# Optimization experiments

Measured on AMD Instinct MI355X. Metric: run time of the kernel, lower is better.

The kernel has to match this reference:

```python
import jax, jax.numpy as jnp
import numpy as np

NUM_ITERATIONS = 3  # matches init kwarg num_iterations
B, R, CIN, COUT, K = 32, 2048, 64, 64, 16


def squash(s):
    # squash along the last (capsule-vector) axis, as in the torch module
    sq = jnp.sum(s * s, axis=-1, keepdims=True)
    return (sq / (1.0 + sq)) * s / jnp.sqrt(sq)


def setup_inputs() -> dict:
    key = jax.random.key(0)
    k1, k2 = jax.random.split(key)
    x = jax.random.normal(k1, (B, R, CIN), dtype=jnp.float32)
    route_weights = jax.random.normal(k2, (K, R, CIN, COUT), dtype=jnp.float32) * 0.05
    return {"x": x, "route_weights": route_weights}


def reference(x, route_weights):
    # priors[k,b,r,o] = sum_c x[b,r,c] * W[k,r,c,o]   -> [K, B, R, COUT]
    priors = jnp.einsum('brc,krco->kbro', x, route_weights)
    logits = jnp.zeros(priors.shape[:3] + (1,), dtype=priors.dtype)  # [K,B,R,1]
    outputs = None
    for i in range(NUM_ITERATIONS):
        probs = jax.nn.softmax(logits, axis=2)  # softmax over route nodes (torch dim=2)
        outputs = squash(jnp.sum(probs * priors, axis=2, keepdims=True))  # [K,B,1,COUT]
        if i != NUM_ITERATIONS - 1:
            logits = logits + jnp.sum(priors * outputs, axis=-1, keepdims=True)
    return outputs[:, :, 0, :]  # [K, B, COUT]
```

## Files before the change

### kernel.cpp

```cpp
#include <hip/hip_runtime.h>
#include <hip/hip_bf16.h>
#include <stdint.h>

#define NB 32
#define NR 2048
#define NC 64
#define NO 64
#define NK 16
#define CHC 8
#define NCHUNK (NC / CHC)

__device__ __forceinline__ uint32_t f2bf(float f) {
  uint32_t u = __builtin_bit_cast(uint32_t, f);
  return (u + 0x7fffu + ((u >> 16) & 1u)) >> 16;
}
__device__ __forceinline__ uint32_t packbf2(float lo, float hi) {
  return f2bf(lo) | (f2bf(hi) << 16);
}

__device__ __forceinline__ void gload_lds16(const float* g, float* l) {
  __builtin_amdgcn_global_load_lds(
      (const __attribute__((address_space(1))) void*)g,
      (__attribute__((address_space(3))) void*)l, 16, 0, 0);
}

__global__ __launch_bounds__(256) void transpose_x(const float* __restrict__ x,
                                                   float* __restrict__ xT) {
  __shared__ float tile[32][65];
  const int r = blockIdx.x, t = threadIdx.x;
  {
    const int b = t >> 3, c0 = (t & 7) << 3;
    const float* xp = x + ((size_t)b * NR + r) * NC + c0;
    float4 v0 = *(const float4*)xp;
    float4 v1 = *(const float4*)(xp + 4);
    tile[b][c0 + 0] = v0.x; tile[b][c0 + 1] = v0.y; tile[b][c0 + 2] = v0.z; tile[b][c0 + 3] = v0.w;
    tile[b][c0 + 4] = v1.x; tile[b][c0 + 5] = v1.y; tile[b][c0 + 6] = v1.z; tile[b][c0 + 7] = v1.w;
  }
  __syncthreads();
  {
    const int c = t >> 2, b0 = (t & 3) << 3;
    float4 w0 = make_float4(tile[b0 + 0][c], tile[b0 + 1][c], tile[b0 + 2][c], tile[b0 + 3][c]);
    float4 w1 = make_float4(tile[b0 + 4][c], tile[b0 + 5][c], tile[b0 + 6][c], tile[b0 + 7][c]);
    float* op = xT + ((size_t)r * NC + c) * NB + b0;
    *(float4*)op = w0;
    *(float4*)(op + 4) = w1;
  }
}

__global__ __launch_bounds__(256, 3) void priors_gemm(const float* __restrict__ xT,
                                                      const float* __restrict__ W,
                                                      __hip_bfloat16* __restrict__ priors) {
  __shared__ float ldsW[2][4][CHC][64];
  __shared__ float ldsX[2][4][CHC][32];
  const int w = threadIdx.x >> 6, lane = threadIdx.x & 63;
  const int bg = lane >> 3, og = lane & 7;
  const int k = blockIdx.x & 15;
  const int rbase = (blockIdx.x >> 4) * 4;
  const int r = rbase + w;

  const float* wsrc = W + ((size_t)(k * NR + rbase + (w >> 1))) * (NC * NO)
                        + (w & 1) * 256 + lane * 4;
  const float* xsrc = xT + ((size_t)r * NC) * NB + lane * 4;

  float acc[4][8] = {};

  auto stage = [&](int t, int buf) {
    const int c0 = t * CHC;
    float* dw = &ldsW[buf][0][0][0] + w * 256;
    gload_lds16(wsrc + c0 * 64, dw);
    gload_lds16(wsrc + (size_t)2 * (NC * NO) + c0 * 64, dw + 1024);
    gload_lds16(xsrc + c0 * 32, &ldsX[buf][0][0][0] + w * 256);
  };

  auto compute = [&](int buf) {
#pragma unroll
    for (int c = 0; c < CHC; ++c) {
      float4 xv = *(const float4*)&ldsX[buf][w][c][bg * 4];
      float4 wa = *(const float4*)&ldsW[buf][w][c][og * 8];
      float4 wb = *(const float4*)&ldsW[buf][w][c][og * 8 + 4];
      float xr[4] = {xv.x, xv.y, xv.z, xv.w};
      float wr[8] = {wa.x, wa.y, wa.z, wa.w, wb.x, wb.y, wb.z, wb.w};
#pragma unroll
      for (int a = 0; a < 4; ++a)
#pragma unroll
        for (int b = 0; b < 8; ++b) acc[a][b] = fmaf(xr[a], wr[b], acc[a][b]);
    }
  };

  stage(0, 0);
  __syncthreads();
#pragma unroll
  for (int t = 0; t < NCHUNK; ++t) {
    if (t + 1 < NCHUNK) stage(t + 1, (t + 1) & 1);
    compute(t & 1);
    __syncthreads();
  }

#pragma unroll
  for (int i = 0; i < 4; ++i) {
    uint4 uv;
    uv.x = packbf2(acc[i][0], acc[i][1]);
    uv.y = packbf2(acc[i][2], acc[i][3]);
    uv.z = packbf2(acc[i][4], acc[i][5]);
    uv.w = packbf2(acc[i][6], acc[i][7]);
    __hip_bfloat16* pp = priors + ((size_t)(k * NR + r) * NB + bg * 4 + i) * NO + og * 8;
    *(uint4*)pp = uv;
  }
}

template <int PASS>
__global__ __launch_bounds__(256) void routing(const __hip_bfloat16* __restrict__ priors,
                                               float* __restrict__ Abuf,
                                               const float* __restrict__ o_prev,
                                               float* __restrict__ o_out) {
  __shared__ float o_lds[64];
  __shared__ float red_num[4][8][8];
  __shared__ float red_den[4];
  const int kb = blockIdx.x;
  const int k = kb >> 5, b = kb & 31;
  const int tid = threadIdx.x, w = tid >> 6, lane = tid & 63;
  const int g = lane >> 3, sl = lane & 7;
  const int rsub = w * 8 + g;
  const __hip_bfloat16* pbase = priors + (size_t)k * NR * NB * NO + (size_t)b * NO;
  float* ab = Abuf + (size_t)kb * NR;

  if (PASS == 1) {
    float sum[8];
#pragma unroll
    for (int j = 0; j < 8; ++j) sum[j] = 0.f;
    for (int it = 0; it < NR / 32; ++it) {
      const int r = it * 32 + rsub;
      uint4 pv = *(const uint4*)(pbase + (size_t)r * (NB * NO) + sl * 8);
      sum[0] += __builtin_bit_cast(float, pv.x << 16);
      sum[1] += __builtin_bit_cast(float, pv.x & 0xffff0000u);
      sum[2] += __builtin_bit_cast(float, pv.y << 16);
      sum[3] += __builtin_bit_cast(float, pv.y & 0xffff0000u);
      sum[4] += __builtin_bit_cast(float, pv.z << 16);
      sum[5] += __builtin_bit_cast(float, pv.z & 0xffff0000u);
      sum[6] += __builtin_bit_cast(float, pv.w << 16);
      sum[7] += __builtin_bit_cast(float, pv.w & 0xffff0000u);
    }
#pragma unroll
    for (int m = 8; m < 64; m <<= 1)
#pragma unroll
      for (int j = 0; j < 8; ++j) sum[j] += __shfl_xor(sum[j], m, 64);
    if (lane < 8) {
#pragma unroll
      for (int j = 0; j < 8; ++j) red_num[w][lane][j] = sum[j];
    }
    __syncthreads();
    if (tid < 64) {
      const int s_ = tid >> 3, j_ = tid & 7;
      float sv = (red_num[0][s_][j_] + red_num[1][s_][j_] +
                  red_num[2][s_][j_] + red_num[3][s_][j_]) * (1.f / (float)NR);
      float sq = sv * sv;
#pragma unroll
      for (int m = 1; m < 64; m <<= 1) sq += __shfl_xor(sq, m, 64);
      o_lds[tid] = (sq / (1.f + sq)) * rsqrtf(sq) * sv;
    }
    __syncthreads();
  } else {
    if (tid < 64) o_lds[tid] = o_prev[kb * 64 + tid];
    __syncthreads();
  }

  float os[8];
#pragma unroll
  for (int j = 0; j < 8; ++j) os[j] = o_lds[sl * 8 + j];

  float num[8];
#pragma unroll
  for (int j = 0; j < 8; ++j) num[j] = 0.f;
  float den = 0.f;

  for (int it = 0; it < NR / 32; ++it) {
    const int r = it * 32 + rsub;
    uint4 pv = *(const uint4*)(pbase + (size_t)r * (NB * NO) + sl * 8);
    float f[8];
    f[0] = __builtin_bit_cast(float, pv.x << 16);
    f[1] = __builtin_bit_cast(float, pv.x & 0xffff0000u);
    f[2] = __builtin_bit_cast(float, pv.y << 16);
    f[3] = __builtin_bit_cast(float, pv.y & 0xffff0000u);
    f[4] = __builtin_bit_cast(float, pv.z << 16);
    f[5] = __builtin_bit_cast(float, pv.z & 0xffff0000u);
    f[6] = __builtin_bit_cast(float, pv.w << 16);
    f[7] = __builtin_bit_cast(float, pv.w & 0xffff0000u);

    float d = 0.f;
#pragma unroll
    for (int j = 0; j < 8; ++j) d = fmaf(f[j], os[j], d);
#pragma unroll
    for (int m = 1; m < 8; m <<= 1) d += __shfl_xor(d, m, 64);

    float lg;
    if (PASS == 1) {
      lg = d;
      if (sl == 0) ab[r] = d;
    } else {
      lg = d + ab[r];
    }
    float e = __expf(lg);
    den += e;
#pragma unroll
    for (int j = 0; j < 8; ++j) num[j] = fmaf(e, f[j], num[j]);
  }

#pragma unroll
  for (int m = 8; m < 64; m <<= 1) {
    den += __shfl_xor(den, m, 64);
#pragma unroll
    for (int j = 0; j < 8; ++j) num[j] += __shfl_xor(num[j], m, 64);
  }
  if (lane < 8) {
#pragma unroll
    for (int j = 0; j < 8; ++j) red_num[w][lane][j] = num[j];
    if (lane == 0) red_den[w] = den;
  }
  __syncthreads();

  if (tid < 64) {
    const int s_ = tid >> 3, j_ = tid & 7;
    float nm = red_num[0][s_][j_] + red_num[1][s_][j_] + red_num[2][s_][j_] + red_num[3][s_][j_];
    float dn = red_den[0] + red_den[1] + red_den[2] + red_den[3];
    float sv = nm / dn;
    float sq = sv * sv;
#pragma unroll
    for (int m = 1; m < 64; m <<= 1) sq += __shfl_xor(sq, m, 64);
    float ov = (sq / (1.f + sq)) * rsqrtf(sq) * sv;
    o_out[kb * 64 + tid] = ov;
  }
}

extern "C" void kernel_launch(void* const* d_in, const int* in_sizes, int n_in,
                              void* d_out, int out_size, void* d_ws, size_t ws_size,
                              hipStream_t stream) {
  const float* x = (const float*)d_in[0];
  const float* W = (const float*)d_in[1];
  float* out = (float*)d_out;
  char* ws = (char*)d_ws;

  size_t off = 0;
  float* xT = (float*)(ws + off);                  off += (size_t)NR * NC * NB * 4;
  __hip_bfloat16* priors = (__hip_bfloat16*)(ws + off); off += (size_t)NK * NB * NR * NO * 2;
  float* o1 = (float*)(ws + off);                  off += (size_t)NK * NB * NO * 4;
  float* Abuf = (float*)(ws + off);                off += (size_t)NK * NB * NR * 4;

  transpose_x<<<NR, 256, 0, stream>>>(x, xT);
  priors_gemm<<<(NR / 4) * NK, 256, 0, stream>>>(xT, W, priors);
  routing<1><<<NK * NB, 256, 0, stream>>>(priors, Abuf, nullptr, o1);
  routing<2><<<NK * NB, 256, 0, stream>>>(priors, Abuf, o1, out);
}
```

Measured before the change: 255.9 us.

## Compute priors with bf16 MFMA instead of scalar FP32 FMAs

The x transpose kernel now writes x pre-converted to bf16 in MFMA A-fragment layout. The priors GEMM is rewritten to stage W rows into LDS, convert them to bf16 B fragments on the fly, and run 16x16x32 bf16 MFMAs, with each wave handling one k and the block looping over 8 route nodes. The intent is to replace scalar FMA throughput with matrix-core throughput, since W is streamed once and the FMA work dominates. It adds bf16 rounding of the inputs, which costs precision, and adds an LDS round-trip epilogue for coalesced stores.

```diff
diff --git a/kernel.cpp b/kernel.cpp
--- a/kernel.cpp
+++ b/kernel.cpp
@@ -7,8 +7,9 @@
 #define NC 64
 #define NO 64
 #define NK 16
-#define CHC 8
-#define NCHUNK (NC / CHC)
+
+using bf16x8 = __attribute__((ext_vector_type(8))) short;
+using f32x4  = __attribute__((ext_vector_type(4))) float;
 
 __device__ __forceinline__ uint32_t f2bf(float f) {
   uint32_t u = __builtin_bit_cast(uint32_t, f);
@@ -24,87 +25,100 @@
       (__attribute__((address_space(3))) void*)l, 16, 0, 0);
 }
 
-__global__ __launch_bounds__(256) void transpose_x(const float* __restrict__ x,
-                                                   float* __restrict__ xT) {
-  __shared__ float tile[32][65];
+__global__ __launch_bounds__(256) void make_xbf(const float* __restrict__ x,
+                                                ushort* __restrict__ xbf) {
+  __shared__ float tile[32][72];
   const int r = blockIdx.x, t = threadIdx.x;
   {
     const int b = t >> 3, c0 = (t & 7) << 3;
     const float* xp = x + ((size_t)b * NR + r) * NC + c0;
-    float4 v0 = *(const float4*)xp;
-    float4 v1 = *(const float4*)(xp + 4);
-    tile[b][c0 + 0] = v0.x; tile[b][c0 + 1] = v0.y; tile[b][c0 + 2] = v0.z; tile[b][c0 + 3] = v0.w;
-    tile[b][c0 + 4] = v1.x; tile[b][c0 + 5] = v1.y; tile[b][c0 + 6] = v1.z; tile[b][c0 + 7] = v1.w;
+    *(float4*)&tile[b][c0] = *(const float4*)xp;
+    *(float4*)&tile[b][c0 + 4] = *(const float4*)(xp + 4);
   }
   __syncthreads();
   {
-    const int c = t >> 2, b0 = (t & 3) << 3;
-    float4 w0 = make_float4(tile[b0 + 0][c], tile[b0 + 1][c], tile[b0 + 2][c], tile[b0 + 3][c]);
-    float4 w1 = make_float4(tile[b0 + 4][c], tile[b0 + 5][c], tile[b0 + 6][c], tile[b0 + 7][c]);
-    float* op = xT + ((size_t)r * NC + c) * NB + b0;
-    *(float4*)op = w0;
-    *(float4*)(op + 4) = w1;
-  }
-}
-
-__global__ __launch_bounds__(256, 3) void priors_gemm(const float* __restrict__ xT,
+    const int ks = t >> 7, mt = (t >> 6) & 1, l = t & 63;
+    const int b = mt * 16 + (l & 15);
+    const int cb = ks * 32 + (l >> 4) * 8;
+    uint4 uv;
+    uv.x = packbf2(tile[b][cb + 0], tile[b][cb + 1]);
+    uv.y = packbf2(tile[b][cb + 2], tile[b][cb + 3]);
+    uv.z = packbf2(tile[b][cb + 4], tile[b][cb + 5]);
+    uv.w = packbf2(tile[b][cb + 6], tile[b][cb + 7]);
+    *(uint4*)(xbf + (size_t)r * 2048 + t * 8) = uv;
+  }
+}
+
+__global__ __launch_bounds__(256, 2) void priors_gemm(const ushort* __restrict__ xbf,
                                                       const float* __restrict__ W,
-                                                      __hip_bfloat16* __restrict__ priors) {
-  __shared__ float ldsW[2][4][CHC][64];
-  __shared__ float ldsX[2][4][CHC][32];
+                                                      ushort* __restrict__ priors) {
+  __shared__ float ldsW[2][4][2048];
   const int w = threadIdx.x >> 6, lane = threadIdx.x & 63;
-  const int bg = lane >> 3, og = lane & 7;
-  const int k = blockIdx.x & 15;
-  const int rbase = (blockIdx.x >> 4) * 4;
-  const int r = rbase + w;
-
-  const float* wsrc = W + ((size_t)(k * NR + rbase + (w >> 1))) * (NC * NO)
-                        + (w & 1) * 256 + lane * 4;
-  const float* xsrc = xT + ((size_t)r * NC) * NB + lane * 4;
-
-  float acc[4][8] = {};
-
-  auto stage = [&](int t, int buf) {
-    const int c0 = t * CHC;
-    float* dw = &ldsW[buf][0][0][0] + w * 256;
-    gload_lds16(wsrc + c0 * 64, dw);
-    gload_lds16(wsrc + (size_t)2 * (NC * NO) + c0 * 64, dw + 1024);
-    gload_lds16(xsrc + c0 * 32, &ldsX[buf][0][0][0] + w * 256);
+  const int g = lane >> 4, col = lane & 15;
+  const int kq = blockIdx.x & 3, rblk = blockIdx.x >> 2;
+  const int k = kq * 4 + w;
+
+  f32x4 acc[2][4];
+
+  auto stage = [&](int rr, int ks, int buf) {
+    const float* src = W + ((size_t)(k * NR + rblk * 8 + rr)) * 4096 + ks * 2048 + lane * 4;
+    float* dst = &ldsW[buf][w][0] + lane * 4;
+#pragma unroll
+    for (int i = 0; i < 8; ++i) gload_lds16(src + i * 256, dst + i * 256);
   };
 
-  auto compute = [&](int buf) {
-#pragma unroll
-    for (int c = 0; c < CHC; ++c) {
-      float4 xv = *(const float4*)&ldsX[buf][w][c][bg * 4];
-      float4 wa = *(const float4*)&ldsW[buf][w][c][og * 8];
-      float4 wb = *(const float4*)&ldsW[buf][w][c][og * 8 + 4];
-      float xr[4] = {xv.x, xv.y, xv.z, xv.w};
-      float wr[8] = {wa.x, wa.y, wa.z, wa.w, wb.x, wb.y, wb.z, wb.w};
-#pragma unroll
-      for (int a = 0; a < 4; ++a)
-#pragma unroll
-        for (int b = 0; b < 8; ++b) acc[a][b] = fmaf(xr[a], wr[b], acc[a][b]);
+  auto compute = [&](int rr, int ks, int buf) {
+    const float* pw = &ldsW[buf][w][0];
+    const size_t r = rblk * 8 + rr;
+    bf16x8 af0 = *(const bf16x8*)(xbf + ((r * 2 + ks) * 2 + 0) * 512 + lane * 8);
+    bf16x8 af1 = *(const bf16x8*)(xbf + ((r * 2 + ks) * 2 + 1) * 512 + lane * 8);
+#pragma unroll
+    for (int nt = 0; nt < 4; ++nt) {
+      float f[8];
+#pragma unroll
+      for (int e = 0; e < 8; ++e) f[e] = pw[(g * 8 + e) * 64 + nt * 16 + col];
+      uint4 uv;
+      uv.x = packbf2(f[0], f[1]);
+      uv.y = packbf2(f[2], f[3]);
+      uv.z = packbf2(f[4], f[5]);
+      uv.w = packbf2(f[6], f[7]);
+      bf16x8 bfr = __builtin_bit_cast(bf16x8, uv);
+      acc[0][nt] = __builtin_amdgcn_mfma_f32_16x16x32_bf16(af0, bfr, acc[0][nt], 0, 0, 0);
+      acc[1][nt] = __builtin_amdgcn_mfma_f32_16x16x32_bf16(af1, bfr, acc[1][nt], 0, 0, 0);
     }
   };
 
-  stage(0, 0);
+  auto epilogue = [&](int rr, int buf) {
+    ushort* ep = (ushort*)&ldsW[buf][w][0];
+#pragma unroll
+    for (int mt = 0; mt < 2; ++mt)
+#pragma unroll
+      for (int nt = 0; nt < 4; ++nt)
+#pragma unroll
+        for (int reg = 0; reg < 4; ++reg)
+          ep[(mt * 16 + g * 4 + reg) * 64 + nt * 16 + col] = (ushort)f2bf(acc[mt][nt][reg]);
+    ushort* pp = priors + ((size_t)(k * NR + rblk * 8 + rr)) * 2048;
+#pragma unroll
+    for (int i = 0; i < 4; ++i) {
+      uint4 v = *(const uint4*)(ep + lane * 8 + i * 512);
+      *(uint4*)(pp + lane * 8 + i * 512) = v;
+    }
+  };
+
+  stage(0, 0, 0);
   __syncthreads();
-#pragma unroll
-  for (int t = 0; t < NCHUNK; ++t) {
-    if (t + 1 < NCHUNK) stage(t + 1, (t + 1) & 1);
-    compute(t & 1);
-    __syncthreads();
-  }
-
-#pragma unroll
-  for (int i = 0; i < 4; ++i) {
-    uint4 uv;
-    uv.x = packbf2(acc[i][0], acc[i][1]);
-    uv.y = packbf2(acc[i][2], acc[i][3]);
-    uv.z = packbf2(acc[i][4], acc[i][5]);
-    uv.w = packbf2(acc[i][6], acc[i][7]);
-    __hip_bfloat16* pp = priors + ((size_t)(k * NR + r) * NB + bg * 4 + i) * NO + og * 8;
-    *(uint4*)pp = uv;
+  for (int ti = 0; ti < 8; ++ti) {
+#pragma unroll
+    for (int mt = 0; mt < 2; ++mt)
+#pragma unroll
+      for (int nt = 0; nt < 4; ++nt) acc[mt][nt] = f32x4{0.f, 0.f, 0.f, 0.f};
+    stage(ti, 1, 1);
+    compute(ti, 0, 0);
+    __syncthreads();
+    if (ti < 7) stage(ti + 1, 0, 0);
+    compute(ti, 1, 1);
+    epilogue(ti, 1);
+    __syncthreads();
   }
 }
 
@@ -240,13 +254,13 @@
   char* ws = (char*)d_ws;
 
   size_t off = 0;
-  float* xT = (float*)(ws + off);                  off += (size_t)NR * NC * NB * 4;
-  __hip_bfloat16* priors = (__hip_bfloat16*)(ws + off); off += (size_t)NK * NB * NR * NO * 2;
+  ushort* xbf = (ushort*)(ws + off);               off += (size_t)NR * 2048 * 2;
+  ushort* priors = (ushort*)(ws + off);            off += (size_t)NK * NR * NB * NO * 2;
   float* o1 = (float*)(ws + off);                  off += (size_t)NK * NB * NO * 4;
   float* Abuf = (float*)(ws + off);                off += (size_t)NK * NB * NR * 4;
 
-  transpose_x<<<NR, 256, 0, stream>>>(x, xT);
-  priors_gemm<<<(NR / 4) * NK, 256, 0, stream>>>(xT, W, priors);
-  routing<1><<<NK * NB, 256, 0, stream>>>(priors, Abuf, nullptr, o1);
-  routing<2><<<NK * NB, 256, 0, stream>>>(priors, Abuf, o1, out);
-}
+  make_xbf<<<NR, 256, 0, stream>>>(x, xbf);
+  priors_gemm<<<(NR / 8) * (NK / 4), 256, 0, stream>>>(xbf, W, priors);
+  routing<1><<<NK * NB, 256, 0, stream>>>((const __hip_bfloat16*)priors, Abuf, nullptr, o1);
+  routing<2><<<NK * NB, 256, 0, stream>>>((const __hip_bfloat16*)priors, Abuf, o1, out);
+}
```

Result: faster. 240.7 us (-6.0%).
